# Kernel tuning notes

Measured on AMD Instinct MI355X. Metric: run time of the kernel, lower is better.

Reference implementation:

```python
import jax, jax.numpy as jnp
import numpy as np

N, IN_F, OUT_F, K = 256, 1024, 128, 32

def setup_inputs() -> dict:
    key = jax.random.key(0)
    k1, k2 = jax.random.split(key)
    x = jax.random.normal(k1, (N, IN_F), dtype=jnp.float32)
    T = jax.random.normal(k2, (IN_F, OUT_F, K), dtype=jnp.float32)
    return {"x": x, "T": T}

def reference(x, T):
    # matrices: [N, OUT_F, K]
    M = jnp.einsum('ni,iok->nok', x, T)
    # pairwise L1 distance over kernel dim: [N, N, OUT_F]
    norm = jnp.abs(M[:, None, :, :] - M[None, :, :, :]).sum(axis=3)
    expnorm = jnp.exp(-norm)
    # sum over the other-sample axis; subtract self-term exp(0)=1
    o_b = expnorm.sum(axis=0) - 1.0  # [N, OUT_F]
    return jnp.concatenate([x, o_b], axis=1)
```

## Files before the change

### kernel.cpp

```cpp
#include <hip/hip_runtime.h>

typedef unsigned short u16;
typedef __attribute__((ext_vector_type(8))) short short8_t;
typedef __attribute__((ext_vector_type(4))) float f32x4;

#define N_SAMP 256
#define IN_F   1024
#define OUT_F  128
#define KDIM   32
#define JTOT   (OUT_F * KDIM)
#define OUT_ROW (IN_F + OUT_F)

#define CHUNKS 8
#define MPC    32
#define MPW    8

__device__ __forceinline__ u16 f2bf(float f) {
    union { float f; unsigned u; } v; v.f = f;
    unsigned r = v.u + 0x7FFFu + ((v.u >> 16) & 1u);
    return (u16)(r >> 16);
}


__global__ __launch_bounds__(256) void prep_kernel(const float* __restrict__ x,
                                                   const float* __restrict__ T,
                                                   float* __restrict__ out,
                                                   u16* __restrict__ At,
                                                   u16* __restrict__ Bt) {
    __shared__ float Ls[64 * 65];
    const int t = threadIdx.x;
    const int j0 = blockIdx.x * 64, k0 = blockIdx.y * 64;
    const int r = t >> 2, c4 = t & 3;

    const float4* src = reinterpret_cast<const float4*>(T + (size_t)(k0 + r) * JTOT + j0 + c4 * 16);
    float4 v0 = src[0], v1 = src[1], v2 = src[2], v3 = src[3];
    float vv[16] = {v0.x,v0.y,v0.z,v0.w, v1.x,v1.y,v1.z,v1.w,
                    v2.x,v2.y,v2.z,v2.w, v3.x,v3.y,v3.z,v3.w};
#pragma unroll
    for (int i = 0; i < 16; ++i) Ls[r * 65 + c4 * 16 + i] = vv[i];
    __syncthreads();

    unsigned pk[8];
#pragma unroll
    for (int i = 0; i < 8; ++i) {
        u16 lo = f2bf(Ls[(c4 * 16 + 2 * i    ) * 65 + r]);
        u16 hi = f2bf(Ls[(c4 * 16 + 2 * i + 1) * 65 + r]);
        pk[i] = (unsigned)lo | ((unsigned)hi << 16);
    }
    uint4* dst = reinterpret_cast<uint4*>(Bt + (size_t)(j0 + r) * IN_F + k0 + c4 * 16);
    dst[0] = make_uint4(pk[0], pk[1], pk[2], pk[3]);
    dst[1] = make_uint4(pk[4], pk[5], pk[6], pk[7]);

    const int bid = blockIdx.y * 64 + blockIdx.x;
    if (bid < N_SAMP) {
        float4 v = reinterpret_cast<const float4*>(x + (size_t)bid * IN_F)[t];
        reinterpret_cast<float4*>(out + (size_t)bid * OUT_ROW)[t] = v;
        ushort4 b;
        b.x = f2bf(v.x); b.y = f2bf(v.y); b.z = f2bf(v.z); b.w = f2bf(v.w);
        reinterpret_cast<ushort4*>(At + (size_t)bid * IN_F)[t] = b;
    }
}

#define LDB 136
__global__ __launch_bounds__(128) void mfma_gemm(const u16* __restrict__ At,
                                                 const u16* __restrict__ Bt,
                                                 float* __restrict__ Mt) {
    __shared__ u16 Bs[2][64 * LDB];
    __shared__ u16 As[2][32 * LDB];
    const int t = threadIdx.x;
    const int w = t >> 6, l = t & 63;
    const int jb = blockIdx.x * 64, nb = blockIdx.y * 32;
    const int rb = t >> 1, hb = t & 1;
    const int ra = t >> 2, qa = t & 3;

    f32x4 acc00 = {0.f,0.f,0.f,0.f}, acc01 = {0.f,0.f,0.f,0.f};
    f32x4 acc10 = {0.f,0.f,0.f,0.f}, acc11 = {0.f,0.f,0.f,0.f};

    float4 sb[8], sa[4];
    auto LOADG = [&](int it) {
        const float4* gb = reinterpret_cast<const float4*>(Bt + (size_t)(jb + rb) * IN_F + it * 128 + hb * 64);
#pragma unroll
        for (int i = 0; i < 8; ++i) sb[i] = gb[i];
        const float4* ga = reinterpret_cast<const float4*>(At + (size_t)(nb + ra) * IN_F + it * 128 + qa * 32);
#pragma unroll
        for (int i = 0; i < 4; ++i) sa[i] = ga[i];
    };
    auto STORE = [&](int b) {
#pragma unroll
        for (int i = 0; i < 8; ++i) *reinterpret_cast<float4*>(&Bs[b][rb * LDB + hb * 64 + i * 8]) = sb[i];
#pragma unroll
        for (int i = 0; i < 4; ++i) *reinterpret_cast<float4*>(&As[b][ra * LDB + qa * 32 + i * 8]) = sa[i];
    };

    LOADG(0); STORE(0); __syncthreads();

#pragma unroll 2
    for (int it = 0; it < 8; ++it) {
        const int cur = it & 1;
        if (it < 7) LOADG(it + 1);
#pragma unroll
        for (int s = 0; s < 4; ++s) {
            const int co = s * 32 + 8 * (l >> 4);
            short8_t a0 = *reinterpret_cast<const short8_t*>(&Bs[cur][(w * 32 +      (l & 15)) * LDB + co]);
            short8_t a1 = *reinterpret_cast<const short8_t*>(&Bs[cur][(w * 32 + 16 + (l & 15)) * LDB + co]);
            short8_t b0 = *reinterpret_cast<const short8_t*>(&As[cur][(          (l & 15)) * LDB + co]);
            short8_t b1 = *reinterpret_cast<const short8_t*>(&As[cur][(     16 + (l & 15)) * LDB + co]);
            acc00 = __builtin_amdgcn_mfma_f32_16x16x32_bf16(a0, b0, acc00, 0, 0, 0);
            acc01 = __builtin_amdgcn_mfma_f32_16x16x32_bf16(a0, b1, acc01, 0, 0, 0);
            acc10 = __builtin_amdgcn_mfma_f32_16x16x32_bf16(a1, b0, acc10, 0, 0, 0);
            acc11 = __builtin_amdgcn_mfma_f32_16x16x32_bf16(a1, b1, acc11, 0, 0, 0);
        }
        if (it < 7) STORE((it + 1) & 1);
        __syncthreads();
    }

    const int jrow = jb + w * 32 + (l >> 4) * 4;
    const int ncol = nb + (l & 15);
#pragma unroll
    for (int r = 0; r < 4; ++r) {
        Mt[(size_t)(jrow + r     ) * N_SAMP + ncol     ] = acc00[r];
        Mt[(size_t)(jrow + r     ) * N_SAMP + ncol + 16] = acc01[r];
        Mt[(size_t)(jrow + 16 + r) * N_SAMP + ncol     ] = acc10[r];
        Mt[(size_t)(jrow + 16 + r) * N_SAMP + ncol + 16] = acc11[r];
    }
}

__global__ __launch_bounds__(256) void dist_part(const float* __restrict__ Mt,
                                                 float* __restrict__ part) {
    __shared__ float Mo[MPC][36];
    __shared__ float Pred[4][N_SAMP];
    const int t = threadIdx.x, w = t >> 6, l = t & 63;
    const int o  = blockIdx.x;
    const int mb = blockIdx.y * MPC;

    {
        const int m = t & 31, kb = (t >> 5) * 4;
#pragma unroll
        for (int kk = 0; kk < 4; ++kk)
            Mo[m][kb + kk] = Mt[(size_t)(o * KDIM + kb + kk) * N_SAMP + mb + m];
    }
    __syncthreads();

    float accd[4][MPW];
#pragma unroll
    for (int r = 0; r < 4; ++r)
#pragma unroll
        for (int m = 0; m < MPW; ++m) accd[r][m] = 0.f;

#pragma unroll
    for (int kh = 0; kh < 4; ++kh) {
        float r0[8], r1[8], r2[8], r3[8];
#pragma unroll
        for (int k = 0; k < 8; ++k) {
            const float* p = Mt + (size_t)(o * KDIM + kh * 8 + k) * N_SAMP + l;
            r0[k] = p[0]; r1[k] = p[64]; r2[k] = p[128]; r3[k] = p[192];
        }
#pragma unroll
        for (int m = 0; m < MPW; ++m) {
            float mo[8];
#pragma unroll
            for (int i = 0; i < 2; ++i)
                *reinterpret_cast<float4*>(&mo[i * 4]) =
                    *reinterpret_cast<const float4*>(&Mo[w * MPW + m][kh * 8 + i * 4]);
#pragma unroll
            for (int k = 0; k < 8; ++k) {
                accd[0][m] += fabsf(r0[k] - mo[k]);
                accd[1][m] += fabsf(r1[k] - mo[k]);
                accd[2][m] += fabsf(r2[k] - mo[k]);
                accd[3][m] += fabsf(r3[k] - mo[k]);
            }
        }
    }

    float a0 = 0.f, a1 = 0.f, a2 = 0.f, a3 = 0.f;
#pragma unroll
    for (int m = 0; m < MPW; ++m) {
        a0 += __expf(-accd[0][m]); a1 += __expf(-accd[1][m]);
        a2 += __expf(-accd[2][m]); a3 += __expf(-accd[3][m]);
    }
    Pred[w][l] = a0; Pred[w][l + 64] = a1; Pred[w][l + 128] = a2; Pred[w][l + 192] = a3;
    __syncthreads();

    {
        float s = Pred[0][t] + Pred[1][t] + Pred[2][t] + Pred[3][t];
        part[(size_t)blockIdx.y * (OUT_F * N_SAMP) + o * N_SAMP + t] = s;
    }
}

__global__ __launch_bounds__(256) void dist_reduce(const float* __restrict__ part,
                                                   float* __restrict__ out) {
    const int o = blockIdx.x, n = threadIdx.x;
    float s = -1.0f;
#pragma unroll
    for (int c = 0; c < CHUNKS; ++c)
        s += part[(size_t)c * (OUT_F * N_SAMP) + o * N_SAMP + n];
    out[(size_t)n * OUT_ROW + IN_F + o] = s;
}

__global__ __launch_bounds__(256) void copy_init_kernel(const float* __restrict__ x,
                                                        float* __restrict__ out) {
    int n = blockIdx.x, t = threadIdx.x;
    reinterpret_cast<float4*>(out + (size_t)n * OUT_ROW)[t] =
        reinterpret_cast<const float4*>(x + (size_t)n * IN_F)[t];
    if (t < OUT_F) out[(size_t)n * OUT_ROW + IN_F + t] = -1.0f;
}

#define BM 64
#define BN 64
#define BK 16
#define AS_STRIDE 68
__global__ __launch_bounds__(256) void gemm_kernel(const float* __restrict__ x,
                                                   const float* __restrict__ T,
                                                   float* __restrict__ M) {
    __shared__ float As_[BK][AS_STRIDE];
    __shared__ float Bs_[BK][BN];
    const int jb = blockIdx.x * BN, nb = blockIdx.y * BM;
    const int t = threadIdx.x, tx = t & 15, ty = t >> 4;
    float acc[4][4] = {};
    for (int k0 = 0; k0 < IN_F; k0 += BK) {
        {
            int row = t >> 2, cg = (t & 3) * 4;
            float4 v = *reinterpret_cast<const float4*>(&x[(size_t)(nb + row) * IN_F + k0 + cg]);
            As_[cg + 0][row] = v.x; As_[cg + 1][row] = v.y;
            As_[cg + 2][row] = v.z; As_[cg + 3][row] = v.w;
        }
        {
            int r = t >> 4, cg = (t & 15) * 4;
            *reinterpret_cast<float4*>(&Bs_[r][cg]) =
                *reinterpret_cast<const float4*>(&T[(size_t)(k0 + r) * JTOT + jb + cg]);
        }
        __syncthreads();
#pragma unroll
        for (int kk = 0; kk < BK; ++kk) {
            float4 av = *reinterpret_cast<const float4*>(&As_[kk][ty * 4]);
            float4 bv = *reinterpret_cast<const float4*>(&Bs_[kk][tx * 4]);
            float a[4] = {av.x, av.y, av.z, av.w}, b[4] = {bv.x, bv.y, bv.z, bv.w};
#pragma unroll
            for (int i = 0; i < 4; ++i)
#pragma unroll
                for (int j = 0; j < 4; ++j) acc[i][j] += a[i] * b[j];
        }
        __syncthreads();
    }
#pragma unroll
    for (int i = 0; i < 4; ++i) {
        int n = nb + ty * 4 + i;
        float4 v = make_float4(acc[i][0], acc[i][1], acc[i][2], acc[i][3]);
        *reinterpret_cast<float4*>(&M[(size_t)n * JTOT + jb + tx * 4]) = v;
    }
}

__global__ __launch_bounds__(256) void dist_kernel(const float* __restrict__ M,
                                                   float* __restrict__ out) {
    __shared__ float Mo_[64][KDIM];
    const int o = blockIdx.x >> 2, chunk = blockIdx.x & 3, t = threadIdx.x;
    float r[KDIM];
    const float4* mrow = reinterpret_cast<const float4*>(&M[(size_t)t * JTOT + o * KDIM]);
#pragma unroll
    for (int f = 0; f < 8; ++f) {
        float4 v = mrow[f];
        r[f*4+0]=v.x; r[f*4+1]=v.y; r[f*4+2]=v.z; r[f*4+3]=v.w;
    }
    const int mbase = chunk * 64;
    {
        int row = t >> 3, f4 = t & 7;
        *reinterpret_cast<float4*>(&Mo_[row][f4*4]) =
            *reinterpret_cast<const float4*>(&M[(size_t)(mbase+row)*JTOT + o*KDIM + f4*4]);
        *reinterpret_cast<float4*>(&Mo_[row+32][f4*4]) =
            *reinterpret_cast<const float4*>(&M[(size_t)(mbase+row+32)*JTOT + o*KDIM + f4*4]);
    }
    __syncthreads();
    float acc = 0.f;
    for (int m = 0; m < 64; ++m) {
        float d = 0.f;
#pragma unroll
        for (int k = 0; k < KDIM; ++k) d += fabsf(r[k] - Mo_[m][k]);
        acc += __expf(-d);
    }
    atomicAdd(&out[(size_t)t * OUT_ROW + IN_F + o], acc);
}

extern "C" void kernel_launch(void* const* d_in, const int* in_sizes, int n_in,
                              void* d_out, int out_size, void* d_ws, size_t ws_size,
                              hipStream_t stream) {
    const float* x = (const float*)d_in[0];
    const float* T = (const float*)d_in[1];
    float* out = (float*)d_out;

    const size_t MT_BYTES = (size_t)JTOT * N_SAMP * 4;
    const size_t AT_BYTES = (size_t)N_SAMP * IN_F * 2;
    const size_t BT_BYTES = (size_t)JTOT * IN_F * 2;

    if (ws_size >= MT_BYTES + AT_BYTES + BT_BYTES) {
        float* Mt = (float*)d_ws;
        u16*   At = (u16*)((char*)d_ws + MT_BYTES);
        u16*   Bt = (u16*)((char*)d_ws + MT_BYTES + AT_BYTES);
        float* part = (float*)Bt;

        prep_kernel<<<dim3(JTOT / 64, IN_F / 64), 256, 0, stream>>>(x, T, out, At, Bt);
        mfma_gemm<<<dim3(JTOT / 64, N_SAMP / 32), 128, 0, stream>>>(At, Bt, Mt);
        dist_part<<<dim3(OUT_F, CHUNKS), 256, 0, stream>>>(Mt, part);
        dist_reduce<<<OUT_F, 256, 0, stream>>>(part, out);
    } else {
        float* M = (float*)d_ws;
        copy_init_kernel<<<N_SAMP, 256, 0, stream>>>(x, out);
        dim3 ggrid(JTOT / BN, N_SAMP / BM);
        gemm_kernel<<<ggrid, 256, 0, stream>>>(x, T, M);
        dist_kernel<<<OUT_F * 4, 256, 0, stream>>>(M, out);
    }
}
```

Before: 117.8 us.

## Fuse bf16 conversion into GEMM with split-K and drop prep kernel

Removes the separate prep kernel that transposed T and converted x/T to bf16, and instead converts fp32 inputs to bf16 on the fly while staging into shared memory inside the GEMM. The GEMM tile grows to 64x64 with 256 threads, and K is split in two across blockIdx.z, writing two partial M buffers that the distance kernel sums when loading. This saves one kernel launch and the bf16 intermediate round-trip, at the cost of reading fp32 T directly (double bytes), scattered 32-bit LDS transpose stores, and doubling the M traffic read by dist_part.

```diff
diff --git a/kernel.cpp b/kernel.cpp
--- a/kernel.cpp
+++ b/kernel.cpp
@@ -10,6 +10,7 @@
 #define KDIM   32
 #define JTOT   (OUT_F * KDIM)
 #define OUT_ROW (IN_F + OUT_F)
+#define MT_ELEMS ((size_t)JTOT * N_SAMP)
 
 #define CHUNKS 8
 #define MPC    32
@@ -22,106 +23,97 @@
 }
 
 
-__global__ __launch_bounds__(256) void prep_kernel(const float* __restrict__ x,
-                                                   const float* __restrict__ T,
-                                                   float* __restrict__ out,
-                                                   u16* __restrict__ At,
-                                                   u16* __restrict__ Bt) {
-    __shared__ float Ls[64 * 65];
-    const int t = threadIdx.x;
-    const int j0 = blockIdx.x * 64, k0 = blockIdx.y * 64;
-    const int r = t >> 2, c4 = t & 3;
-
-    const float4* src = reinterpret_cast<const float4*>(T + (size_t)(k0 + r) * JTOT + j0 + c4 * 16);
-    float4 v0 = src[0], v1 = src[1], v2 = src[2], v3 = src[3];
-    float vv[16] = {v0.x,v0.y,v0.z,v0.w, v1.x,v1.y,v1.z,v1.w,
-                    v2.x,v2.y,v2.z,v2.w, v3.x,v3.y,v3.z,v3.w};
-#pragma unroll
-    for (int i = 0; i < 16; ++i) Ls[r * 65 + c4 * 16 + i] = vv[i];
-    __syncthreads();
-
-    unsigned pk[8];
-#pragma unroll
-    for (int i = 0; i < 8; ++i) {
-        u16 lo = f2bf(Ls[(c4 * 16 + 2 * i    ) * 65 + r]);
-        u16 hi = f2bf(Ls[(c4 * 16 + 2 * i + 1) * 65 + r]);
-        pk[i] = (unsigned)lo | ((unsigned)hi << 16);
-    }
-    uint4* dst = reinterpret_cast<uint4*>(Bt + (size_t)(j0 + r) * IN_F + k0 + c4 * 16);
-    dst[0] = make_uint4(pk[0], pk[1], pk[2], pk[3]);
-    dst[1] = make_uint4(pk[4], pk[5], pk[6], pk[7]);
-
-    const int bid = blockIdx.y * 64 + blockIdx.x;
-    if (bid < N_SAMP) {
-        float4 v = reinterpret_cast<const float4*>(x + (size_t)bid * IN_F)[t];
-        reinterpret_cast<float4*>(out + (size_t)bid * OUT_ROW)[t] = v;
-        ushort4 b;
-        b.x = f2bf(v.x); b.y = f2bf(v.y); b.z = f2bf(v.z); b.w = f2bf(v.w);
-        reinterpret_cast<ushort4*>(At + (size_t)bid * IN_F)[t] = b;
-    }
-}
-
 #define LDB 136
-__global__ __launch_bounds__(128) void mfma_gemm(const u16* __restrict__ At,
-                                                 const u16* __restrict__ Bt,
-                                                 float* __restrict__ Mt) {
+__global__ __launch_bounds__(256) void gemm_fused(const float* __restrict__ x,
+                                                  const float* __restrict__ T,
+                                                  float* __restrict__ out,
+                                                  float* __restrict__ Mt) {
     __shared__ u16 Bs[2][64 * LDB];
-    __shared__ u16 As[2][32 * LDB];
-    const int t = threadIdx.x;
-    const int w = t >> 6, l = t & 63;
-    const int jb = blockIdx.x * 64, nb = blockIdx.y * 32;
-    const int rb = t >> 1, hb = t & 1;
-    const int ra = t >> 2, qa = t & 3;
+    __shared__ u16 As[2][64 * LDB];
+    const int t = threadIdx.x, w = t >> 6, l = t & 63;
+    const int wr = (w >> 1) * 32, wc = (w & 1) * 32;
+    const int jb = blockIdx.x * 64, nb = blockIdx.y * 64;
+    const int kbase = blockIdx.z * 512;
+    float* Mth = Mt + (size_t)blockIdx.z * MT_ELEMS;
+
+    if (blockIdx.z == 0 && blockIdx.x < 16) {
+        const int row = nb + blockIdx.x * 4 + (t >> 6);
+        const float4* src = reinterpret_cast<const float4*>(x + (size_t)row * IN_F);
+        float4* dst = reinterpret_cast<float4*>(out + (size_t)row * OUT_ROW);
+#pragma unroll
+        for (int i = 0; i < 4; ++i) dst[(t & 63) + 64 * i] = src[(t & 63) + 64 * i];
+    }
+
+    const int kp = t >> 2;
+    const int q  = t & 3;
 
     f32x4 acc00 = {0.f,0.f,0.f,0.f}, acc01 = {0.f,0.f,0.f,0.f};
     f32x4 acc10 = {0.f,0.f,0.f,0.f}, acc11 = {0.f,0.f,0.f,0.f};
 
-    float4 sb[8], sa[4];
+    float4 ta[4], tb[4], xv[8];
     auto LOADG = [&](int it) {
-        const float4* gb = reinterpret_cast<const float4*>(Bt + (size_t)(jb + rb) * IN_F + it * 128 + hb * 64);
-#pragma unroll
-        for (int i = 0; i < 8; ++i) sb[i] = gb[i];
-        const float4* ga = reinterpret_cast<const float4*>(At + (size_t)(nb + ra) * IN_F + it * 128 + qa * 32);
-#pragma unroll
-        for (int i = 0; i < 4; ++i) sa[i] = ga[i];
+        const int k0 = kbase + it * 128;
+        const float4* gT0 = reinterpret_cast<const float4*>(T + (size_t)(k0 + 2 * kp    ) * JTOT + jb + q * 16);
+        const float4* gT1 = reinterpret_cast<const float4*>(T + (size_t)(k0 + 2 * kp + 1) * JTOT + jb + q * 16);
+#pragma unroll
+        for (int i = 0; i < 4; ++i) { ta[i] = gT0[i]; tb[i] = gT1[i]; }
+        const float4* gx = reinterpret_cast<const float4*>(x + (size_t)(nb + kp) * IN_F + k0 + q * 32);
+#pragma unroll
+        for (int i = 0; i < 8; ++i) xv[i] = gx[i];
     };
     auto STORE = [&](int b) {
 #pragma unroll
-        for (int i = 0; i < 8; ++i) *reinterpret_cast<float4*>(&Bs[b][rb * LDB + hb * 64 + i * 8]) = sb[i];
-#pragma unroll
-        for (int i = 0; i < 4; ++i) *reinterpret_cast<float4*>(&As[b][ra * LDB + qa * 32 + i * 8]) = sa[i];
+        for (int i = 0; i < 4; ++i) {
+            const float* fa = reinterpret_cast<const float*>(&ta[i]);
+            const float* fb = reinterpret_cast<const float*>(&tb[i]);
+#pragma unroll
+            for (int c = 0; c < 4; ++c) {
+                unsigned v = (unsigned)f2bf(fa[c]) | ((unsigned)f2bf(fb[c]) << 16);
+                *reinterpret_cast<unsigned*>(&Bs[b][(q * 16 + i * 4 + c) * LDB + 2 * kp]) = v;
+            }
+        }
+#pragma unroll
+        for (int i = 0; i < 4; ++i) {
+            const float* f0 = reinterpret_cast<const float*>(&xv[2 * i]);
+            const float* f1 = reinterpret_cast<const float*>(&xv[2 * i + 1]);
+            uint4 pv;
+            pv.x = (unsigned)f2bf(f0[0]) | ((unsigned)f2bf(f0[1]) << 16);
+            pv.y = (unsigned)f2bf(f0[2]) | ((unsigned)f2bf(f0[3]) << 16);
+            pv.z = (unsigned)f2bf(f1[0]) | ((unsigned)f2bf(f1[1]) << 16);
+            pv.w = (unsigned)f2bf(f1[2]) | ((unsigned)f2bf(f1[3]) << 16);
+            *reinterpret_cast<uint4*>(&As[b][kp * LDB + q * 32 + i * 8]) = pv;
+        }
     };
 
     LOADG(0); STORE(0); __syncthreads();
 
-#pragma unroll 2
-    for (int it = 0; it < 8; ++it) {
+    for (int it = 0; it < 4; ++it) {
         const int cur = it & 1;
-        if (it < 7) LOADG(it + 1);
+        if (it < 3) LOADG(it + 1);
 #pragma unroll
         for (int s = 0; s < 4; ++s) {
             const int co = s * 32 + 8 * (l >> 4);
-            short8_t a0 = *reinterpret_cast<const short8_t*>(&Bs[cur][(w * 32 +      (l & 15)) * LDB + co]);
-            short8_t a1 = *reinterpret_cast<const short8_t*>(&Bs[cur][(w * 32 + 16 + (l & 15)) * LDB + co]);
-            short8_t b0 = *reinterpret_cast<const short8_t*>(&As[cur][(          (l & 15)) * LDB + co]);
-            short8_t b1 = *reinterpret_cast<const short8_t*>(&As[cur][(     16 + (l & 15)) * LDB + co]);
+            short8_t a0 = *reinterpret_cast<const short8_t*>(&Bs[cur][(wr +      (l & 15)) * LDB + co]);
+            short8_t a1 = *reinterpret_cast<const short8_t*>(&Bs[cur][(wr + 16 + (l & 15)) * LDB + co]);
+            short8_t b0 = *reinterpret_cast<const short8_t*>(&As[cur][(wc +      (l & 15)) * LDB + co]);
+            short8_t b1 = *reinterpret_cast<const short8_t*>(&As[cur][(wc + 16 + (l & 15)) * LDB + co]);
             acc00 = __builtin_amdgcn_mfma_f32_16x16x32_bf16(a0, b0, acc00, 0, 0, 0);
             acc01 = __builtin_amdgcn_mfma_f32_16x16x32_bf16(a0, b1, acc01, 0, 0, 0);
             acc10 = __builtin_amdgcn_mfma_f32_16x16x32_bf16(a1, b0, acc10, 0, 0, 0);
             acc11 = __builtin_amdgcn_mfma_f32_16x16x32_bf16(a1, b1, acc11, 0, 0, 0);
         }
-        if (it < 7) STORE((it + 1) & 1);
+        if (it < 3) STORE(cur ^ 1);
         __syncthreads();
     }
 
-    const int jrow = jb + w * 32 + (l >> 4) * 4;
-    const int ncol = nb + (l & 15);
+    const int jrow = jb + wr + (l >> 4) * 4;
+    const int ncol = nb + wc + (l & 15);
 #pragma unroll
     for (int r = 0; r < 4; ++r) {
-        Mt[(size_t)(jrow + r     ) * N_SAMP + ncol     ] = acc00[r];
-        Mt[(size_t)(jrow + r     ) * N_SAMP + ncol + 16] = acc01[r];
-        Mt[(size_t)(jrow + 16 + r) * N_SAMP + ncol     ] = acc10[r];
-        Mt[(size_t)(jrow + 16 + r) * N_SAMP + ncol + 16] = acc11[r];
+        Mth[(size_t)(jrow + r     ) * N_SAMP + ncol     ] = acc00[r];
+        Mth[(size_t)(jrow + r     ) * N_SAMP + ncol + 16] = acc01[r];
+        Mth[(size_t)(jrow + 16 + r) * N_SAMP + ncol     ] = acc10[r];
+        Mth[(size_t)(jrow + 16 + r) * N_SAMP + ncol + 16] = acc11[r];
     }
 }
 
@@ -132,12 +124,15 @@
     const int t = threadIdx.x, w = t >> 6, l = t & 63;
     const int o  = blockIdx.x;
     const int mb = blockIdx.y * MPC;
+    const float* Mt1 = Mt + MT_ELEMS;
 
     {
         const int m = t & 31, kb = (t >> 5) * 4;
 #pragma unroll
-        for (int kk = 0; kk < 4; ++kk)
-            Mo[m][kb + kk] = Mt[(size_t)(o * KDIM + kb + kk) * N_SAMP + mb + m];
+        for (int kk = 0; kk < 4; ++kk) {
+            size_t idx = (size_t)(o * KDIM + kb + kk) * N_SAMP + mb + m;
+            Mo[m][kb + kk] = Mt[idx] + Mt1[idx];
+        }
     }
     __syncthreads();
 
@@ -152,8 +147,13 @@
         float r0[8], r1[8], r2[8], r3[8];
 #pragma unroll
         for (int k = 0; k < 8; ++k) {
-            const float* p = Mt + (size_t)(o * KDIM + kh * 8 + k) * N_SAMP + l;
-            r0[k] = p[0]; r1[k] = p[64]; r2[k] = p[128]; r3[k] = p[192];
+            const size_t off = (size_t)(o * KDIM + kh * 8 + k) * N_SAMP + l;
+            const float* p0 = Mt  + off;
+            const float* p1 = Mt1 + off;
+            r0[k] = p0[0]   + p1[0];
+            r1[k] = p0[64]  + p1[64];
+            r2[k] = p0[128] + p1[128];
+            r3[k] = p0[192] + p1[192];
         }
 #pragma unroll
         for (int m = 0; m < MPW; ++m) {
@@ -287,18 +287,13 @@
     const float* T = (const float*)d_in[1];
     float* out = (float*)d_out;
 
-    const size_t MT_BYTES = (size_t)JTOT * N_SAMP * 4;
-    const size_t AT_BYTES = (size_t)N_SAMP * IN_F * 2;
-    const size_t BT_BYTES = (size_t)JTOT * IN_F * 2;
-
-    if (ws_size >= MT_BYTES + AT_BYTES + BT_BYTES) {
-        float* Mt = (float*)d_ws;
-        u16*   At = (u16*)((char*)d_ws + MT_BYTES);
-        u16*   Bt = (u16*)((char*)d_ws + MT_BYTES + AT_BYTES);
-        float* part = (float*)Bt;
-
-        prep_kernel<<<dim3(JTOT / 64, IN_F / 64), 256, 0, stream>>>(x, T, out, At, Bt);
-        mfma_gemm<<<dim3(JTOT / 64, N_SAMP / 32), 128, 0, stream>>>(At, Bt, Mt);
+    const size_t NEED = 2 * MT_ELEMS * 4 + (size_t)CHUNKS * OUT_F * N_SAMP * 4;
+
+    if (ws_size >= NEED) {
+        float* Mt   = (float*)d_ws;
+        float* part = Mt + 2 * MT_ELEMS;
+
+        gemm_fused<<<dim3(JTOT / 64, N_SAMP / 64, 2), 256, 0, stream>>>(x, T, out, Mt);
         dist_part<<<dim3(OUT_F, CHUNKS), 256, 0, stream>>>(Mt, part);
         dist_reduce<<<OUT_F, 256, 0, stream>>>(part, out);
     } else {
```

Measured after the change: 103.4 us. 12.3% less time.
